# Optimization experiments

Hardware: AMD Instinct MI355X
Metric: run time of the kernel (lower is better)

The kernel has to match this reference:

```python
import jax, jax.numpy as jnp
import numpy as np

NEG_INF = -1e9  # matches torch masked_fill value -1000000000.0


def setup_inputs() -> dict:
    key = jax.random.key(0)
    ks = jax.random.split(key, 7)
    B, S = 16, 4096
    scale = 1.0 / np.sqrt(S)  # keep linear outputs O(1) like torch init
    return {
        "x": jax.random.normal(ks[0], (B, S), dtype=jnp.float32),
        "Wq": jax.random.normal(ks[1], (S, S), dtype=jnp.float32) * scale,
        "bq": jax.random.normal(ks[2], (S,), dtype=jnp.float32) * scale,
        "Wk": jax.random.normal(ks[3], (S, S), dtype=jnp.float32) * scale,
        "bk": jax.random.normal(ks[4], (S,), dtype=jnp.float32) * scale,
        "Wv": jax.random.normal(ks[5], (S, S), dtype=jnp.float32) * scale,
        "bv": jax.random.normal(ks[6], (S,), dtype=jnp.float32) * scale,
    }


def reference(x, Wq, bq, Wk, bk, Wv, bv):
    # x: [B, S]; torch Linear: y = x @ W.T + b with W [out, in]
    q = x @ Wq.T + bq  # [B, S]
    k = x @ Wk.T + bk  # [B, S]
    v = x @ Wv.T + bv  # [B, S]
    # d=1 attention: scores[b,i,j] = q[b,i] * k[b,j]  -> outer product
    scores = q[:, :, None] * k[:, None, :]  # [B, S, S]
    S = x.shape[1]
    causal = jnp.tril(jnp.ones((S, S), dtype=bool))  # mask=True path
    scores = jnp.where(causal, scores, NEG_INF)
    attn = jax.nn.softmax(scores, axis=-1)  # [B, S, S]
    out = jnp.einsum("bij,bj->bi", attn, v)  # [B, S]
    return out
```

## Files before the change

### kernel.cpp

```cpp
#include <hip/hip_runtime.h>
#include <math.h>

#define S 4096
#define B 16
#define SC 512
#define R 8

__global__ __launch_bounds__(256) void qkv_kernel(
    const float* __restrict__ x,
    const float* __restrict__ Wq, const float* __restrict__ bq,
    const float* __restrict__ Wk, const float* __restrict__ bk,
    const float* __restrict__ Wv, const float* __restrict__ bv,
    float* __restrict__ q, float* __restrict__ k, float* __restrict__ v)
{
    __shared__ float xs[B][SC];
    const int tid  = threadIdx.x;
    const int lane = tid & 63;
    const int wave = tid >> 6;
    const int bx   = blockIdx.x;
    const int mat  = bx >> 8;
    const int obase = (bx & 255) * 16;

    const float* W    = (mat == 0) ? Wq : (mat == 1) ? Wk : Wv;
    const float* bias = (mat == 0) ? bq : (mat == 1) ? bk : bv;
    float*       out  = (mat == 0) ? q  : (mat == 1) ? k  : v;
    const int o0 = obase + wave * 4;

    float acc[4][16];
    #pragma unroll
    for (int oi = 0; oi < 4; ++oi)
        #pragma unroll
        for (int b = 0; b < 16; ++b) acc[oi][b] = 0.f;

    for (int c = 0; c < S / SC; ++c) {
        __syncthreads();
        #pragma unroll
        for (int r = 0; r < (B * SC / 4) / 256; ++r) {
            int f4 = tid + r * 256;
            int b  = f4 / (SC / 4);
            int s4 = f4 % (SC / 4);
            float4 xv = *(const float4*)&x[b * S + c * SC + s4 * 4];
            *(float4*)&xs[b][s4 * 4] = xv;
        }
        __syncthreads();
        #pragma unroll
        for (int it = 0; it < SC / 256; ++it) {
            const int sl = it * 256 + lane * 4;
            const int sg = c * SC + sl;
            float4 w0 = *(const float4*)&W[(size_t)(o0 + 0) * S + sg];
            float4 w1 = *(const float4*)&W[(size_t)(o0 + 1) * S + sg];
            float4 w2 = *(const float4*)&W[(size_t)(o0 + 2) * S + sg];
            float4 w3 = *(const float4*)&W[(size_t)(o0 + 3) * S + sg];
            #pragma unroll
            for (int b = 0; b < 16; ++b) {
                float4 xv = *(const float4*)&xs[b][sl];
                acc[0][b] = fmaf(w0.x, xv.x, acc[0][b]);
                acc[0][b] = fmaf(w0.y, xv.y, acc[0][b]);
                acc[0][b] = fmaf(w0.z, xv.z, acc[0][b]);
                acc[0][b] = fmaf(w0.w, xv.w, acc[0][b]);
                acc[1][b] = fmaf(w1.x, xv.x, acc[1][b]);
                acc[1][b] = fmaf(w1.y, xv.y, acc[1][b]);
                acc[1][b] = fmaf(w1.z, xv.z, acc[1][b]);
                acc[1][b] = fmaf(w1.w, xv.w, acc[1][b]);
                acc[2][b] = fmaf(w2.x, xv.x, acc[2][b]);
                acc[2][b] = fmaf(w2.y, xv.y, acc[2][b]);
                acc[2][b] = fmaf(w2.z, xv.z, acc[2][b]);
                acc[2][b] = fmaf(w2.w, xv.w, acc[2][b]);
                acc[3][b] = fmaf(w3.x, xv.x, acc[3][b]);
                acc[3][b] = fmaf(w3.y, xv.y, acc[3][b]);
                acc[3][b] = fmaf(w3.z, xv.z, acc[3][b]);
                acc[3][b] = fmaf(w3.w, xv.w, acc[3][b]);
            }
        }
    }

    #pragma unroll
    for (int oi = 0; oi < 4; ++oi) {
        #pragma unroll
        for (int b = 0; b < 16; ++b) {
            float s = acc[oi][b];
            #pragma unroll
            for (int off = 32; off; off >>= 1) s += __shfl_xor(s, off, 64);
            if (lane == oi * 16 + b)
                out[b * S + o0 + oi] = s + bias[o0 + oi];
        }
    }
}

__global__ __launch_bounds__(256) void scan_kernel(
    const float* __restrict__ k,
    float* __restrict__ rmax, float* __restrict__ rmin)
{
    __shared__ float smax[256], smin[256];
    const int b = blockIdx.x, t = threadIdx.x;
    const float* kb = k + b * S;

    float seg[16];
    float lmax = -INFINITY, lmin = INFINITY;
    #pragma unroll
    for (int e = 0; e < 16; ++e) {
        seg[e] = kb[t * 16 + e];
        lmax = fmaxf(lmax, seg[e]);
        lmin = fminf(lmin, seg[e]);
    }
    smax[t] = lmax; smin[t] = lmin;
    __syncthreads();
    for (int off = 1; off < 256; off <<= 1) {
        float vx = (t >= off) ? smax[t - off] : -INFINITY;
        float vn = (t >= off) ? smin[t - off] :  INFINITY;
        __syncthreads();
        smax[t] = fmaxf(smax[t], vx);
        smin[t] = fminf(smin[t], vn);
        __syncthreads();
    }
    float runmax = (t > 0) ? smax[t - 1] : -INFINITY;
    float runmin = (t > 0) ? smin[t - 1] :  INFINITY;
    #pragma unroll
    for (int e = 0; e < 16; ++e) {
        runmax = fmaxf(runmax, seg[e]);
        runmin = fminf(runmin, seg[e]);
        rmax[b * S + t * 16 + e] = runmax;
        rmin[b * S + t * 16 + e] = runmin;
    }
}

__global__ __launch_bounds__(256) void attn_kernel(
    const float* __restrict__ q, const float* __restrict__ k,
    const float* __restrict__ v,
    const float* __restrict__ rmax, const float* __restrict__ rmin,
    float* __restrict__ out)
{
    const int tid = threadIdx.x, lane = tid & 63, wave = tid >> 6;
    const int task = blockIdx.x * 4 + wave;
    const int b    = task & 15;
    const int rbi  = task >> 4;
    const int i0   = (511 - rbi) * R;
    const float* kb = k + b * S;
    const float* vb = v + b * S;
    const float LOG2E = 1.4426950408889634f;

    float a[R], cc[R], den[R], num[R];
    #pragma unroll
    for (int r = 0; r < R; ++r) {
        float qi = q[b * S + i0 + r];
        float m  = (qi >= 0.f) ? qi * rmax[b * S + i0 + r]
                               : qi * rmin[b * S + i0 + r];
        a[r]  = qi * LOG2E;
        cc[r] = -m * LOG2E;
        den[r] = 0.f; num[r] = 0.f;
    }

    const int nfull = (i0 + 1) >> 8;
    for (int it = 0; it < nfull; ++it) {
        const int j = it * 256 + lane * 4;
        float4 k4 = *(const float4*)&kb[j];
        float4 v4 = *(const float4*)&vb[j];
        #pragma unroll
        for (int jj = 0; jj < 4; ++jj) {
            float kx = (&k4.x)[jj], vx = (&v4.x)[jj];
            #pragma unroll
            for (int r = 0; r < R; ++r) {
                float e = exp2f(fmaf(a[r], kx, cc[r]));
                den[r] += e;
                num[r] = fmaf(e, vx, num[r]);
            }
        }
    }
    const int imax = i0 + R - 1;
    for (int j = nfull * 256 + lane; j <= imax; j += 64) {
        float kx = kb[j], vx = vb[j];
        #pragma unroll
        for (int r = 0; r < R; ++r) {
            float e = (j <= i0 + r) ? exp2f(fmaf(a[r], kx, cc[r])) : 0.f;
            den[r] += e;
            num[r] = fmaf(e, vx, num[r]);
        }
    }

    #pragma unroll
    for (int r = 0; r < R; ++r) {
        float d = den[r], n = num[r];
        #pragma unroll
        for (int off = 32; off; off >>= 1) {
            d += __shfl_xor(d, off, 64);
            n += __shfl_xor(n, off, 64);
        }
        if (lane == r) out[b * S + i0 + r] = n / d;
    }
}

extern "C" void kernel_launch(void* const* d_in, const int* in_sizes, int n_in,
                              void* d_out, int out_size, void* d_ws, size_t ws_size,
                              hipStream_t stream) {
    const float* x  = (const float*)d_in[0];
    const float* Wq = (const float*)d_in[1];
    const float* bq = (const float*)d_in[2];
    const float* Wk = (const float*)d_in[3];
    const float* bk = (const float*)d_in[4];
    const float* Wv = (const float*)d_in[5];
    const float* bv = (const float*)d_in[6];
    float* out = (float*)d_out;

    float* ws   = (float*)d_ws;
    float* q    = ws;
    float* k    = ws + 65536;
    float* v    = ws + 131072;
    float* rmax = ws + 196608;
    float* rmin = ws + 262144;

    qkv_kernel<<<768, 256, 0, stream>>>(x, Wq, bq, Wk, bk, Wv, bv, q, k, v);
    scan_kernel<<<16, 256, 0, stream>>>(k, rmax, rmin);
    attn_kernel<<<2048, 256, 0, stream>>>(q, k, v, rmax, rmin, out);
}
```

Baseline: 117.0 us.

## Restructure QKV GEMV tiling: drop LDS staging, prefetch weights, split batch

The QKV projection kernel no longer stages x in shared memory with block barriers. Each wave now computes 8 output rows for 8 batch rows, with the batch split across two blocks, reads x straight from global/L2, and software-prefetches the next chunk of weight rows into registers. The aim is to remove barrier stalls and raise memory-level parallelism when streaming the weights. In exchange, each weight row is read by two blocks (relying on L2 to absorb the duplicate traffic), x is re-read from cache by every wave, and register pressure rises under a launch bound of 3 blocks.

```diff
diff --git a/kernel.cpp b/kernel.cpp
--- a/kernel.cpp
+++ b/kernel.cpp
@@ -3,86 +3,76 @@
 
 #define S 4096
 #define B 16
-#define SC 512
 #define R 8
 
-__global__ __launch_bounds__(256) void qkv_kernel(
+__global__ __launch_bounds__(256, 3) void qkv_kernel(
     const float* __restrict__ x,
     const float* __restrict__ Wq, const float* __restrict__ bq,
     const float* __restrict__ Wk, const float* __restrict__ bk,
     const float* __restrict__ Wv, const float* __restrict__ bv,
     float* __restrict__ q, float* __restrict__ k, float* __restrict__ v)
 {
-    __shared__ float xs[B][SC];
     const int tid  = threadIdx.x;
     const int lane = tid & 63;
     const int wave = tid >> 6;
     const int bx   = blockIdx.x;
     const int mat  = bx >> 8;
-    const int obase = (bx & 255) * 16;
+    const int rem  = bx & 255;
+    const int og   = rem >> 1;
+    const int bh   = rem & 1;
 
     const float* W    = (mat == 0) ? Wq : (mat == 1) ? Wk : Wv;
     const float* bias = (mat == 0) ? bq : (mat == 1) ? bk : bv;
     float*       out  = (mat == 0) ? q  : (mat == 1) ? k  : v;
-    const int o0 = obase + wave * 4;
-
-    float acc[4][16];
-    #pragma unroll
-    for (int oi = 0; oi < 4; ++oi)
-        #pragma unroll
-        for (int b = 0; b < 16; ++b) acc[oi][b] = 0.f;
-
-    for (int c = 0; c < S / SC; ++c) {
-        __syncthreads();
-        #pragma unroll
-        for (int r = 0; r < (B * SC / 4) / 256; ++r) {
-            int f4 = tid + r * 256;
-            int b  = f4 / (SC / 4);
-            int s4 = f4 % (SC / 4);
-            float4 xv = *(const float4*)&x[b * S + c * SC + s4 * 4];
-            *(float4*)&xs[b][s4 * 4] = xv;
-        }
-        __syncthreads();
-        #pragma unroll
-        for (int it = 0; it < SC / 256; ++it) {
-            const int sl = it * 256 + lane * 4;
-            const int sg = c * SC + sl;
-            float4 w0 = *(const float4*)&W[(size_t)(o0 + 0) * S + sg];
-            float4 w1 = *(const float4*)&W[(size_t)(o0 + 1) * S + sg];
-            float4 w2 = *(const float4*)&W[(size_t)(o0 + 2) * S + sg];
-            float4 w3 = *(const float4*)&W[(size_t)(o0 + 3) * S + sg];
-            #pragma unroll
-            for (int b = 0; b < 16; ++b) {
-                float4 xv = *(const float4*)&xs[b][sl];
-                acc[0][b] = fmaf(w0.x, xv.x, acc[0][b]);
-                acc[0][b] = fmaf(w0.y, xv.y, acc[0][b]);
-                acc[0][b] = fmaf(w0.z, xv.z, acc[0][b]);
-                acc[0][b] = fmaf(w0.w, xv.w, acc[0][b]);
-                acc[1][b] = fmaf(w1.x, xv.x, acc[1][b]);
-                acc[1][b] = fmaf(w1.y, xv.y, acc[1][b]);
-                acc[1][b] = fmaf(w1.z, xv.z, acc[1][b]);
-                acc[1][b] = fmaf(w1.w, xv.w, acc[1][b]);
-                acc[2][b] = fmaf(w2.x, xv.x, acc[2][b]);
-                acc[2][b] = fmaf(w2.y, xv.y, acc[2][b]);
-                acc[2][b] = fmaf(w2.z, xv.z, acc[2][b]);
-                acc[2][b] = fmaf(w2.w, xv.w, acc[2][b]);
-                acc[3][b] = fmaf(w3.x, xv.x, acc[3][b]);
-                acc[3][b] = fmaf(w3.y, xv.y, acc[3][b]);
-                acc[3][b] = fmaf(w3.z, xv.z, acc[3][b]);
-                acc[3][b] = fmaf(w3.w, xv.w, acc[3][b]);
+    const int o0 = og * 32 + wave * 8;
+
+    const float* Wr[8];
+    #pragma unroll
+    for (int r = 0; r < 8; ++r) Wr[r] = W + (size_t)(o0 + r) * S;
+    const float* xb = x + (size_t)(bh * 8) * S;
+
+    float acc[8][8];
+    #pragma unroll
+    for (int r = 0; r < 8; ++r)
+        #pragma unroll
+        for (int bi = 0; bi < 8; ++bi) acc[r][bi] = 0.f;
+
+    float4 wc[8];
+    #pragma unroll
+    for (int r = 0; r < 8; ++r) wc[r] = *(const float4*)&Wr[r][lane * 4];
+
+    for (int it = 0; it < 16; ++it) {
+        float4 wn[8];
+        if (it < 15) {
+            const int sg = (it + 1) * 256 + lane * 4;
+            #pragma unroll
+            for (int r = 0; r < 8; ++r) wn[r] = *(const float4*)&Wr[r][sg];
+        }
+        const int sl = it * 256 + lane * 4;
+        #pragma unroll
+        for (int bi = 0; bi < 8; ++bi) {
+            float4 xv = *(const float4*)&xb[(size_t)bi * S + sl];
+            #pragma unroll
+            for (int r = 0; r < 8; ++r) {
+                acc[r][bi] = fmaf(wc[r].x, xv.x, acc[r][bi]);
+                acc[r][bi] = fmaf(wc[r].y, xv.y, acc[r][bi]);
+                acc[r][bi] = fmaf(wc[r].z, xv.z, acc[r][bi]);
+                acc[r][bi] = fmaf(wc[r].w, xv.w, acc[r][bi]);
             }
         }
-    }
-
-    #pragma unroll
-    for (int oi = 0; oi < 4; ++oi) {
-        #pragma unroll
-        for (int b = 0; b < 16; ++b) {
-            float s = acc[oi][b];
+        #pragma unroll
+        for (int r = 0; r < 8; ++r) wc[r] = wn[r];
+    }
+
+    #pragma unroll
+    for (int r = 0; r < 8; ++r) {
+        #pragma unroll
+        for (int bi = 0; bi < 8; ++bi) {
+            float s = acc[r][bi];
             #pragma unroll
             for (int off = 32; off; off >>= 1) s += __shfl_xor(s, off, 64);
-            if (lane == oi * 16 + b)
-                out[b * S + o0 + oi] = s + bias[o0 + oi];
+            if (lane == r * 8 + bi)
+                out[(size_t)(bh * 8 + bi) * S + o0 + r] = s + bias[o0 + r];
         }
     }
 }
```

Result: slower. 142.9 us (+22.2%).
